# Optimization experiments

Hardware: AMD Instinct MI355X
Metric: run time of the kernel (lower is better)

## Reference

```python
import jax, jax.numpy as jnp
import numpy as np

B, S, D = 4, 2048, 512
H, DK = 16, 32  # n_heads, d_k == d_v == args.mid_dim


def setup_inputs() -> dict:
    key = jax.random.key(0)
    ks = jax.random.split(key, 9)
    s = 0.02
    return {
        "x": jax.random.normal(ks[0], (B, S, D), dtype=jnp.float32),
        "Wq": jax.random.normal(ks[1], (D, H * DK), dtype=jnp.float32) * s,
        "bq": jnp.zeros((H * DK,), dtype=jnp.float32),
        "Wk": jax.random.normal(ks[2], (D, H * DK), dtype=jnp.float32) * s,
        "bk": jnp.zeros((H * DK,), dtype=jnp.float32),
        "Wv": jax.random.normal(ks[3], (D, H * DK), dtype=jnp.float32) * s,
        "bv": jnp.zeros((H * DK,), dtype=jnp.float32),
        "Wo": jax.random.normal(ks[4], (H * DK, D), dtype=jnp.float32) * s,
        "bo": jnp.zeros((D,), dtype=jnp.float32),
        "mask_border": 64,
    }


def reference(x, Wq, bq, Wk, bk, Wv, bv, Wo, bo, mask_border):
    b, s, d = x.shape
    # band mask: tril(ones, border) * triu(ones, -border) == 1 where |i-j| <= border
    i = jnp.arange(s)
    band = (jnp.abs(i[:, None] - i[None, :]) <= mask_border).astype(x.dtype)  # [S,S]

    q = (x @ Wq + bq).reshape(b, s, H, DK)
    k = (x @ Wk + bk).reshape(b, s, H, DK)
    v = (x @ Wv + bv).reshape(b, s, H, DK)

    scale = 1.0 / jnp.sqrt(jnp.asarray(DK, x.dtype))
    # float attn_mask is ADDED to scores (PatchTST-style _ScaledDotProductAttention)
    scores = jnp.einsum("bihd,bjhd->bhij", q, k) * scale + band[None, None]
    attn = jax.nn.softmax(scores, axis=-1)
    o = jnp.einsum("bhij,bjhd->bihd", attn, v).reshape(b, s, H * DK)
    out_1 = o @ Wo + bo  # [B,S,D]

    # reconstruction score + quantiles (side stats; do not feed returned tensor)
    rec_score = jnp.mean((out_1 - x) ** 2, axis=2)  # [B,S]
    q1, q2, q3 = jnp.quantile(rec_score, jnp.array([0.25, 0.5, 0.75], rec_score.dtype), axis=-1)
    del q1, q2, q3

    # tmp = out_1 - x; out_1 = x + tmp  (identity); module returns out_1
    return out_1
```

## Files before the change

### kernel.cpp

```cpp
#include <hip/hip_runtime.h>
#include <hip/hip_bf16.h>

#define B_ 4
#define S_ 2048
#define D_ 512
#define H_ 16
#define DK_ 32
#define MS_ 8192

typedef unsigned short u16;
typedef __attribute__((ext_vector_type(4))) unsigned short u16x4;
typedef __attribute__((ext_vector_type(8))) short bf16x8;
typedef __attribute__((ext_vector_type(4))) float f32x4;

__device__ __forceinline__ u16 f2b(float f) {
    union { float f; unsigned u; } uf; uf.f = f;
    unsigned u = uf.u;
    unsigned r = u + 0x7fffu + ((u >> 16) & 1u);
    return (u16)(r >> 16);
}

__device__ __forceinline__ unsigned cvt_pk_bf16(float lo, float hi) {
    unsigned r;
    asm("v_cvt_pk_bf16_f32 %0, %1, %2" : "=v"(r) : "v"(lo), "v"(hi));
    return r;
}

__device__ __forceinline__ void gload16(const u16* src, u16* dst) {
    __builtin_amdgcn_global_load_lds(
        (const __attribute__((address_space(1))) unsigned int*)src,
        (__attribute__((address_space(3))) unsigned int*)dst, 16, 0, 0);
}

__global__ void cast_f32_to_bf16(const float* __restrict__ in, u16* __restrict__ out, int n4) {
    int i = blockIdx.x * blockDim.x + threadIdx.x;
    if (i >= n4) return;
    f32x4 v = *(const f32x4*)(in + (size_t)i * 4);
    u16x4 o;
    o[0] = f2b(v[0]); o[1] = f2b(v[1]); o[2] = f2b(v[2]); o[3] = f2b(v[3]);
    *(u16x4*)(out + (size_t)i * 4) = o;
}

__global__ void transpose_cast(const float* __restrict__ Wq, const float* __restrict__ Wk,
                               const float* __restrict__ Wv, const float* __restrict__ Wo,
                               u16* __restrict__ out) {
    const int z = blockIdx.z;
    const float* W = (z == 0) ? Wq : (z == 1) ? Wk : (z == 2) ? Wv : Wo;
    u16* O = out + (size_t)z * D_ * D_;
    __shared__ float T[32][33];
    const int n0 = blockIdx.x * 32, k0 = blockIdx.y * 32;
    const int tx = threadIdx.x & 31, ty = threadIdx.x >> 5;
#pragma unroll
    for (int i = 0; i < 4; i++) {
        int row = ty + 8 * i;
        T[tx][row] = W[(size_t)(k0 + row) * D_ + n0 + tx];
    }
    __syncthreads();
#pragma unroll
    for (int i = 0; i < 4; i++) {
        int row = ty + 8 * i;
        O[(size_t)(n0 + row) * D_ + k0 + tx] = f2b(T[row][tx]);
    }
}

__launch_bounds__(256)
__global__ void gemm_qkv(const u16* __restrict__ Xb, const u16* __restrict__ WT,
                         const float* __restrict__ bq, const float* __restrict__ bk, const float* __restrict__ bv,
                         u16* __restrict__ Qw, u16* __restrict__ Kw, u16* __restrict__ Vw) {
    const int which = blockIdx.z;
    const u16* Wt = WT + (size_t)which * D_ * D_;
    const float* bias = (which == 0) ? bq : (which == 1) ? bk : bv;
    u16* Out = (which == 0) ? Qw : (which == 1) ? Kw : Vw;

    __shared__ __attribute__((aligned(16))) u16 As[128][64];
    __shared__ __attribute__((aligned(16))) u16 Bs[128][64];

    const int tid = threadIdx.x;
    const int lane = tid & 63, w = tid >> 6;
    const int wr = w >> 1, wc = w & 1;
    const int g = lane >> 4, c = lane & 15;
    const int bm0 = blockIdx.y * 128, bn0 = blockIdx.x * 128;

    const int trow = tid >> 3;
    const int tcg = (tid & 7) ^ (trow & 7);
    const u16* gA = Xb + (size_t)(bm0 + trow) * D_ + 8 * tcg;
    const u16* gB = Wt + (size_t)(bn0 + trow) * D_ + 8 * tcg;

    f32x4 acc[4][4];
#pragma unroll
    for (int i = 0; i < 4; i++)
#pragma unroll
        for (int j = 0; j < 4; j++) acc[i][j] = (f32x4)0.0f;

    for (int k0 = 0; k0 < D_; k0 += 64) {
#pragma unroll
        for (int i = 0; i < 4; i++) {
            gload16(gA + (size_t)(32 * i) * D_ + k0, &As[0][0] + 512 * w + 2048 * i);
            gload16(gB + (size_t)(32 * i) * D_ + k0, &Bs[0][0] + 512 * w + 2048 * i);
        }
        __syncthreads();
#pragma unroll
        for (int kk = 0; kk < 2; kk++) {
            bf16x8 a[4], b[4];
#pragma unroll
            for (int mi = 0; mi < 4; mi++)
                a[mi] = *(const bf16x8*)&As[wr * 64 + 16 * mi + c][8 * ((4 * kk + g) ^ (c & 7))];
#pragma unroll
            for (int ni = 0; ni < 4; ni++)
                b[ni] = *(const bf16x8*)&Bs[wc * 64 + 16 * ni + c][8 * ((4 * kk + g) ^ (c & 7))];
#pragma unroll
            for (int mi = 0; mi < 4; mi++)
#pragma unroll
                for (int ni = 0; ni < 4; ni++)
                    acc[mi][ni] = __builtin_amdgcn_mfma_f32_16x16x32_bf16(a[mi], b[ni], acc[mi][ni], 0, 0, 0);
        }
        __syncthreads();
    }
#pragma unroll
    for (int mi = 0; mi < 4; mi++)
#pragma unroll
        for (int ni = 0; ni < 4; ni++)
#pragma unroll
            for (int r = 0; r < 4; r++) {
                int m = bm0 + wr * 64 + 16 * mi + 4 * g + r;
                int n = bn0 + wc * 64 + 16 * ni + c;
                float v = acc[mi][ni][r] + bias[n];
                int b = m >> 11, s = m & 2047;
                int h = n >> 5, dk = n & 31;
                Out[(((size_t)(b * H_ + h) * S_) + s) * DK_ + dk] = f2b(v);
            }
}

__launch_bounds__(512)
__global__ void attn_kernel(const u16* __restrict__ Q, const u16* __restrict__ K,
                            const u16* __restrict__ V, u16* __restrict__ O,
                            const int* __restrict__ mbp) {
    const int border = *mbp;
    const unsigned b2u = (unsigned)(2 * border);
    const int bh = blockIdx.x;
    const int q0 = blockIdx.y * 128;
    const int tid = threadIdx.x;
    const int lane = tid & 63;
    const int w = __builtin_amdgcn_readfirstlane(tid >> 6);
    const int g = lane >> 4, c = lane & 15;

    __shared__ __attribute__((aligned(16))) u16 Ks[128][32];
    __shared__ __attribute__((aligned(16))) u16 Vt0[32][68];
    __shared__ __attribute__((aligned(16))) u16 Vt1[32][68];

    const u16* Qbh = Q + (size_t)bh * S_ * DK_;
    const u16* Kbh = K + (size_t)bh * S_ * DK_;
    const u16* Vbh = V + (size_t)bh * S_ * DK_;

    const int qw0 = q0 + w * 16;
    const int qi = qw0 + c;
    const bf16x8 qf = *(const bf16x8*)&Qbh[(size_t)qi * DK_ + 8 * g];

    f32x4 accO[2];
    accO[0] = (f32x4)0.0f; accO[1] = (f32x4)0.0f;
    float lr0 = 0.f, lr1 = 0.f, lr2 = 0.f, lr3 = 0.f;

    const float C1 = (float)(1.4426950408889634 / 5.656854249492381);
    const float C2 = 1.4426950408889634f;

    const int skk = tid >> 3;
    const int sc4 = (tid & 7) << 2;
    const int srow = 32 * ((skk >> 2) & 1) + 16 * ((skk >> 5) & 1) + (((skk >> 3) & 3) << 2) + (skk & 3);

    for (int kv0 = 0; kv0 < S_; kv0 += 128) {
        *(u16x4*)&Ks[srow][sc4]      = *(const u16x4*)&Kbh[(size_t)(kv0 + skk) * DK_ + sc4];
        *(u16x4*)&Ks[64 + srow][sc4] = *(const u16x4*)&Kbh[(size_t)(kv0 + 64 + skk) * DK_ + sc4];
        u16x4 va = *(const u16x4*)&Vbh[(size_t)(kv0 + skk) * DK_ + sc4];
        u16x4 vb = *(const u16x4*)&Vbh[(size_t)(kv0 + 64 + skk) * DK_ + sc4];
#pragma unroll
        for (int j = 0; j < 4; j++) {
            Vt0[sc4 + j][skk] = va[j];
            Vt1[sc4 + j][skk] = vb[j];
        }
        __syncthreads();

        union { unsigned u[4]; bf16x8 v; } pb[4];

        {
            f32x4 sf[4];
#pragma unroll
            for (int ct = 0; ct < 4; ct++) {
                const bf16x8 kf = *(const bf16x8*)&Ks[16 * ct + c][8 * g];
                sf[ct] = __builtin_amdgcn_mfma_f32_16x16x32_bf16(kf, qf, (f32x4)0.0f, 0, 0, 0);
            }
            const int kvs = kv0;
            float e[4][4];
            const bool aOut = (qw0 > kvs + 63 + border) || (qw0 + 15 + border < kvs);
            const bool aIn  = (qw0 + 15 <= kvs + border) && (kvs + 63 <= qw0 + border);
            if (aOut) {
#pragma unroll
                for (int ct = 0; ct < 4; ct++)
#pragma unroll
                    for (int r = 0; r < 4; r++)
                        e[ct][r] = __builtin_amdgcn_exp2f(sf[ct][r] * C1);
            } else if (aIn) {
#pragma unroll
                for (int ct = 0; ct < 4; ct++)
#pragma unroll
                    for (int r = 0; r < 4; r++)
                        e[ct][r] = __builtin_amdgcn_exp2f(__builtin_fmaf(sf[ct][r], C1, C2));
            } else {
                const int qb = qi + border - kvs;
#pragma unroll
                for (int ct = 0; ct < 4; ct++) {
                    const int k0l = 32 * (ct & 1) + 8 * g + 4 * (ct >> 1);
#pragma unroll
                    for (int r = 0; r < 4; r++) {
                        float a = ((unsigned)(qb - (k0l + r)) <= b2u) ? C2 : 0.0f;
                        e[ct][r] = __builtin_amdgcn_exp2f(__builtin_fmaf(sf[ct][r], C1, a));
                    }
                }
            }
#pragma unroll
            for (int ct = 0; ct < 4; ct++) {
                lr0 += e[ct][0]; lr1 += e[ct][1]; lr2 += e[ct][2]; lr3 += e[ct][3];
            }
            pb[0].u[0] = cvt_pk_bf16(e[0][0], e[0][1]);
            pb[0].u[1] = cvt_pk_bf16(e[0][2], e[0][3]);
            pb[0].u[2] = cvt_pk_bf16(e[2][0], e[2][1]);
            pb[0].u[3] = cvt_pk_bf16(e[2][2], e[2][3]);
            pb[1].u[0] = cvt_pk_bf16(e[1][0], e[1][1]);
            pb[1].u[1] = cvt_pk_bf16(e[1][2], e[1][3]);
            pb[1].u[2] = cvt_pk_bf16(e[3][0], e[3][1]);
            pb[1].u[3] = cvt_pk_bf16(e[3][2], e[3][3]);
        }

        {
            f32x4 sf[4];
#pragma unroll
            for (int ct = 0; ct < 4; ct++) {
                const bf16x8 kf = *(const bf16x8*)&Ks[64 + 16 * ct + c][8 * g];
                sf[ct] = __builtin_amdgcn_mfma_f32_16x16x32_bf16(kf, qf, (f32x4)0.0f, 0, 0, 0);
            }
            const int kvs = kv0 + 64;
            float e[4][4];
            const bool aOut = (qw0 > kvs + 63 + border) || (qw0 + 15 + border < kvs);
            const bool aIn  = (qw0 + 15 <= kvs + border) && (kvs + 63 <= qw0 + border);
            if (aOut) {
#pragma unroll
                for (int ct = 0; ct < 4; ct++)
#pragma unroll
                    for (int r = 0; r < 4; r++)
                        e[ct][r] = __builtin_amdgcn_exp2f(sf[ct][r] * C1);
            } else if (aIn) {
#pragma unroll
                for (int ct = 0; ct < 4; ct++)
#pragma unroll
                    for (int r = 0; r < 4; r++)
                        e[ct][r] = __builtin_amdgcn_exp2f(__builtin_fmaf(sf[ct][r], C1, C2));
            } else {
                const int qb = qi + border - kvs;
#pragma unroll
                for (int ct = 0; ct < 4; ct++) {
                    const int k0l = 32 * (ct & 1) + 8 * g + 4 * (ct >> 1);
#pragma unroll
                    for (int r = 0; r < 4; r++) {
                        float a = ((unsigned)(qb - (k0l + r)) <= b2u) ? C2 : 0.0f;
                        e[ct][r] = __builtin_amdgcn_exp2f(__builtin_fmaf(sf[ct][r], C1, a));
                    }
                }
            }
#pragma unroll
            for (int ct = 0; ct < 4; ct++) {
                lr0 += e[ct][0]; lr1 += e[ct][1]; lr2 += e[ct][2]; lr3 += e[ct][3];
            }
            pb[2].u[0] = cvt_pk_bf16(e[0][0], e[0][1]);
            pb[2].u[1] = cvt_pk_bf16(e[0][2], e[0][3]);
            pb[2].u[2] = cvt_pk_bf16(e[2][0], e[2][1]);
            pb[2].u[3] = cvt_pk_bf16(e[2][2], e[2][3]);
            pb[3].u[0] = cvt_pk_bf16(e[1][0], e[1][1]);
            pb[3].u[1] = cvt_pk_bf16(e[1][2], e[1][3]);
            pb[3].u[2] = cvt_pk_bf16(e[3][0], e[3][1]);
            pb[3].u[3] = cvt_pk_bf16(e[3][2], e[3][3]);
        }

#pragma unroll
        for (int t = 0; t < 2; t++) {
            union { u16x4 h[2]; bf16x8 v; } vf;
            vf.h[0] = *(const u16x4*)&Vt0[16 * t + c][8 * g];
            vf.h[1] = *(const u16x4*)&Vt0[16 * t + c][8 * g + 4];
            accO[t] = __builtin_amdgcn_mfma_f32_16x16x32_bf16(vf.v, pb[0].v, accO[t], 0, 0, 0);
            vf.h[0] = *(const u16x4*)&Vt0[16 * t + c][32 + 8 * g];
            vf.h[1] = *(const u16x4*)&Vt0[16 * t + c][32 + 8 * g + 4];
            accO[t] = __builtin_amdgcn_mfma_f32_16x16x32_bf16(vf.v, pb[1].v, accO[t], 0, 0, 0);
            vf.h[0] = *(const u16x4*)&Vt1[16 * t + c][8 * g];
            vf.h[1] = *(const u16x4*)&Vt1[16 * t + c][8 * g + 4];
            accO[t] = __builtin_amdgcn_mfma_f32_16x16x32_bf16(vf.v, pb[2].v, accO[t], 0, 0, 0);
            vf.h[0] = *(const u16x4*)&Vt1[16 * t + c][32 + 8 * g];
            vf.h[1] = *(const u16x4*)&Vt1[16 * t + c][32 + 8 * g + 4];
            accO[t] = __builtin_amdgcn_mfma_f32_16x16x32_bf16(vf.v, pb[3].v, accO[t], 0, 0, 0);
        }
        __syncthreads();
    }

    float l = ((lr0 + lr1) + (lr2 + lr3));
    l += __shfl_xor(l, 16);
    l += __shfl_xor(l, 32);
    const float linv = 1.0f / l;

    const int b = bh >> 4, h = bh & 15;
#pragma unroll
    for (int t = 0; t < 2; t++) {
        u16x4 o4;
#pragma unroll
        for (int r = 0; r < 4; r++) o4[r] = f2b(accO[t][r] * linv);
        *(u16x4*)&O[((size_t)(b * S_ + qi) * H_ + h) * DK_ + 16 * t + 4 * g] = o4;
    }
}

__launch_bounds__(256)
__global__ void gemm_out(const u16* __restrict__ Ob, const u16* __restrict__ WoT,
                         const float* __restrict__ bo, float* __restrict__ out) {
    __shared__ __attribute__((aligned(16))) u16 As[128][64];
    __shared__ __attribute__((aligned(16))) u16 Bs[128][64];

    const int tid = threadIdx.x;
    const int lane = tid & 63, w = tid >> 6;
    const int wr = w >> 1, wc = w & 1;
    const int g = lane >> 4, c = lane & 15;
    const int bm0 = blockIdx.y * 128, bn0 = blockIdx.x * 128;

    const int trow = tid >> 3;
    const int tcg = (tid & 7) ^ (trow & 7);
    const u16* gA = Ob + (size_t)(bm0 + trow) * D_ + 8 * tcg;
    const u16* gB = WoT + (size_t)(bn0 + trow) * D_ + 8 * tcg;

    f32x4 acc[4][4];
#pragma unroll
    for (int i = 0; i < 4; i++)
#pragma unroll
        for (int j = 0; j < 4; j++) acc[i][j] = (f32x4)0.0f;

    for (int k0 = 0; k0 < D_; k0 += 64) {
#pragma unroll
        for (int i = 0; i < 4; i++) {
            gload16(gA + (size_t)(32 * i) * D_ + k0, &As[0][0] + 512 * w + 2048 * i);
            gload16(gB + (size_t)(32 * i) * D_ + k0, &Bs[0][0] + 512 * w + 2048 * i);
        }
        __syncthreads();
#pragma unroll
        for (int kk = 0; kk < 2; kk++) {
            bf16x8 a[4], b[4];
#pragma unroll
            for (int mi = 0; mi < 4; mi++)
                a[mi] = *(const bf16x8*)&As[wr * 64 + 16 * mi + c][8 * ((4 * kk + g) ^ (c & 7))];
#pragma unroll
            for (int ni = 0; ni < 4; ni++)
                b[ni] = *(const bf16x8*)&Bs[wc * 64 + 16 * ni + c][8 * ((4 * kk + g) ^ (c & 7))];
#pragma unroll
            for (int mi = 0; mi < 4; mi++)
#pragma unroll
                for (int ni = 0; ni < 4; ni++)
                    acc[mi][ni] = __builtin_amdgcn_mfma_f32_16x16x32_bf16(a[mi], b[ni], acc[mi][ni], 0, 0, 0);
        }
        __syncthreads();
    }
#pragma unroll
    for (int mi = 0; mi < 4; mi++)
#pragma unroll
        for (int ni = 0; ni < 4; ni++)
#pragma unroll
            for (int r = 0; r < 4; r++) {
                int m = bm0 + wr * 64 + 16 * mi + 4 * g + r;
                int n = bn0 + wc * 64 + 16 * ni + c;
                out[(size_t)m * D_ + n] = acc[mi][ni][r] + bo[n];
            }
}

extern "C" void kernel_launch(void* const* d_in, const int* in_sizes, int n_in,
                              void* d_out, int out_size, void* d_ws, size_t ws_size,
                              hipStream_t stream) {
    const float* x  = (const float*)d_in[0];
    const float* Wq = (const float*)d_in[1];
    const float* bq = (const float*)d_in[2];
    const float* Wk = (const float*)d_in[3];
    const float* bk = (const float*)d_in[4];
    const float* Wv = (const float*)d_in[5];
    const float* bv = (const float*)d_in[6];
    const float* Wo = (const float*)d_in[7];
    const float* bo = (const float*)d_in[8];
    const int* mb   = (const int*)d_in[9];
    float* out = (float*)d_out;

    char* p = (char*)d_ws;
    u16* xb = (u16*)p; p += (size_t)MS_ * D_ * 2;
    u16* wt = (u16*)p; p += (size_t)4 * D_ * D_ * 2;
    u16* qw = (u16*)p; p += (size_t)MS_ * D_ * 2;
    u16* kw = (u16*)p; p += (size_t)MS_ * D_ * 2;
    u16* vw = (u16*)p; p += (size_t)MS_ * D_ * 2;
    u16* ow = (u16*)p; p += (size_t)MS_ * D_ * 2;

    cast_f32_to_bf16<<<4096, 256, 0, stream>>>(x, xb, MS_ * D_ / 4);
    transpose_cast<<<dim3(16, 16, 4), 256, 0, stream>>>(Wq, Wk, Wv, Wo, wt);

    gemm_qkv<<<dim3(4, 64, 3), 256, 0, stream>>>(xb, wt, bq, bk, bv, qw, kw, vw);
    attn_kernel<<<dim3(64, 16), 512, 0, stream>>>(qw, kw, vw, ow, mb);
    gemm_out<<<dim3(4, 64), 256, 0, stream>>>(ow, wt + (size_t)3 * D_ * D_, bo, out);
}
```

Baseline: 116.5 us.

## Process two query tiles per wave, fold softmax scale into Q, sum rows via MFMA

Each attention wave now handles 32 queries instead of 16, so every K/V tile loaded into LDS is reused across twice as many queries, and the grid is halved. The softmax scale times log2(e) is folded into the Q projection epilogue, which removes a multiply per score. Row sums are computed with an MFMA against a ones vector instead of scalar adds and cross-lane shuffles. In exchange, register pressure per wave goes up, there are half as many blocks (512) to fill the GPU, and the row sum is now taken over bf16-rounded probabilities.

```diff
diff --git a/kernel.cpp b/kernel.cpp
--- a/kernel.cpp
+++ b/kernel.cpp
@@ -12,6 +12,8 @@
 typedef __attribute__((ext_vector_type(4))) unsigned short u16x4;
 typedef __attribute__((ext_vector_type(8))) short bf16x8;
 typedef __attribute__((ext_vector_type(4))) float f32x4;
+
+union pbu { unsigned u[4]; bf16x8 v; };
 
 __device__ __forceinline__ u16 f2b(float f) {
     union { float f; unsigned u; } uf; uf.f = f;
@@ -71,6 +73,7 @@
     const u16* Wt = WT + (size_t)which * D_ * D_;
     const float* bias = (which == 0) ? bq : (which == 1) ? bk : bv;
     u16* Out = (which == 0) ? Qw : (which == 1) ? Kw : Vw;
+    const float oscale = (which == 0) ? (float)(1.4426950408889634 / 5.656854249492381) : 1.0f;
 
     __shared__ __attribute__((aligned(16))) u16 As[128][64];
     __shared__ __attribute__((aligned(16))) u16 Bs[128][64];
@@ -124,7 +127,7 @@
             for (int r = 0; r < 4; r++) {
                 int m = bm0 + wr * 64 + 16 * mi + 4 * g + r;
                 int n = bn0 + wc * 64 + 16 * ni + c;
-                float v = acc[mi][ni][r] + bias[n];
+                float v = (acc[mi][ni][r] + bias[n]) * oscale;
                 int b = m >> 11, s = m & 2047;
                 int h = n >> 5, dk = n & 31;
                 Out[(((size_t)(b * H_ + h) * S_) + s) * DK_ + dk] = f2b(v);
@@ -138,34 +141,106 @@
     const int border = *mbp;
     const unsigned b2u = (unsigned)(2 * border);
     const int bh = blockIdx.x;
-    const int q0 = blockIdx.y * 128;
+    const int q0 = blockIdx.y * 256;
     const int tid = threadIdx.x;
     const int lane = tid & 63;
     const int w = __builtin_amdgcn_readfirstlane(tid >> 6);
     const int g = lane >> 4, c = lane & 15;
 
     __shared__ __attribute__((aligned(16))) u16 Ks[128][32];
-    __shared__ __attribute__((aligned(16))) u16 Vt0[32][68];
-    __shared__ __attribute__((aligned(16))) u16 Vt1[32][68];
+    __shared__ __attribute__((aligned(16))) u16 Vt[2][32][68];
 
     const u16* Qbh = Q + (size_t)bh * S_ * DK_;
     const u16* Kbh = K + (size_t)bh * S_ * DK_;
     const u16* Vbh = V + (size_t)bh * S_ * DK_;
 
-    const int qw0 = q0 + w * 16;
-    const int qi = qw0 + c;
-    const bf16x8 qf = *(const bf16x8*)&Qbh[(size_t)qi * DK_ + 8 * g];
-
-    f32x4 accO[2];
-    accO[0] = (f32x4)0.0f; accO[1] = (f32x4)0.0f;
-    float lr0 = 0.f, lr1 = 0.f, lr2 = 0.f, lr3 = 0.f;
-
-    const float C1 = (float)(1.4426950408889634 / 5.656854249492381);
+    const int qw0 = q0 + w * 32;
+    const int qiA = qw0 + c;
+    const int qiB = qw0 + 16 + c;
+    const bf16x8 qfA = *(const bf16x8*)&Qbh[(size_t)qiA * DK_ + 8 * g];
+    const bf16x8 qfB = *(const bf16x8*)&Qbh[(size_t)qiB * DK_ + 8 * g];
+
+    f32x4 accO[2][2];
+    f32x4 accL[2];
+#pragma unroll
+    for (int i = 0; i < 2; i++) { accO[i][0] = (f32x4)0.0f; accO[i][1] = (f32x4)0.0f; accL[i] = (f32x4)0.0f; }
+
     const float C2 = 1.4426950408889634f;
+
+    union { u16x4 h[2]; bf16x8 v; } ones;
+#pragma unroll
+    for (int j = 0; j < 4; j++) { ones.h[0][j] = 0x3F80; ones.h[1][j] = 0x3F80; }
 
     const int skk = tid >> 3;
     const int sc4 = (tid & 7) << 2;
     const int srow = 32 * ((skk >> 2) & 1) + 16 * ((skk >> 5) & 1) + (((skk >> 3) & 3) << 2) + (skk & 3);
+
+    auto sm_pack = [&](const f32x4* sf, int qs0, int qiv, int kvs, pbu* pb) {
+        float e[4][4];
+        const bool aOut = (qs0 > kvs + 63 + border) || (qs0 + 15 + border < kvs);
+        const bool aIn  = (qs0 + 15 <= kvs + border) && (kvs + 63 <= qs0 + border);
+        if (aOut) {
+#pragma unroll
+            for (int ct = 0; ct < 4; ct++)
+#pragma unroll
+                for (int r = 0; r < 4; r++)
+                    e[ct][r] = __builtin_amdgcn_exp2f(sf[ct][r]);
+        } else if (aIn) {
+#pragma unroll
+            for (int ct = 0; ct < 4; ct++)
+#pragma unroll
+                for (int r = 0; r < 4; r++)
+                    e[ct][r] = __builtin_amdgcn_exp2f(sf[ct][r] + C2);
+        } else {
+            const int qb = qiv + border - kvs;
+#pragma unroll
+            for (int ct = 0; ct < 4; ct++) {
+                const int k0l = 32 * (ct & 1) + 8 * g + 4 * (ct >> 1);
+#pragma unroll
+                for (int r = 0; r < 4; r++) {
+                    float a = ((unsigned)(qb - (k0l + r)) <= b2u) ? C2 : 0.0f;
+                    e[ct][r] = __builtin_amdgcn_exp2f(sf[ct][r] + a);
+                }
+            }
+        }
+        pb[0].u[0] = cvt_pk_bf16(e[0][0], e[0][1]);
+        pb[0].u[1] = cvt_pk_bf16(e[0][2], e[0][3]);
+        pb[0].u[2] = cvt_pk_bf16(e[2][0], e[2][1]);
+        pb[0].u[3] = cvt_pk_bf16(e[2][2], e[2][3]);
+        pb[1].u[0] = cvt_pk_bf16(e[1][0], e[1][1]);
+        pb[1].u[1] = cvt_pk_bf16(e[1][2], e[1][3]);
+        pb[1].u[2] = cvt_pk_bf16(e[3][0], e[3][1]);
+        pb[1].u[3] = cvt_pk_bf16(e[3][2], e[3][3]);
+    };
+
+    auto do_sub = [&](int sub, int kvs) {
+        f32x4 sA[4], sB[4];
+#pragma unroll
+        for (int ct = 0; ct < 4; ct++) {
+            const bf16x8 kf = *(const bf16x8*)&Ks[sub * 64 + 16 * ct + c][8 * g];
+            sA[ct] = __builtin_amdgcn_mfma_f32_16x16x32_bf16(kf, qfA, (f32x4)0.0f, 0, 0, 0);
+            sB[ct] = __builtin_amdgcn_mfma_f32_16x16x32_bf16(kf, qfB, (f32x4)0.0f, 0, 0, 0);
+        }
+        pbu pA[2], pB[2];
+        sm_pack(sA, qw0, qiA, kvs, pA);
+        sm_pack(sB, qw0 + 16, qiB, kvs, pB);
+#pragma unroll
+        for (int t2 = 0; t2 < 2; t2++) {
+#pragma unroll
+            for (int ksl = 0; ksl < 2; ksl++) {
+                union { u16x4 h[2]; bf16x8 v; } vf;
+                vf.h[0] = *(const u16x4*)&Vt[sub][16 * t2 + c][32 * ksl + 8 * g];
+                vf.h[1] = *(const u16x4*)&Vt[sub][16 * t2 + c][32 * ksl + 8 * g + 4];
+                accO[0][t2] = __builtin_amdgcn_mfma_f32_16x16x32_bf16(vf.v, pA[ksl].v, accO[0][t2], 0, 0, 0);
+                accO[1][t2] = __builtin_amdgcn_mfma_f32_16x16x32_bf16(vf.v, pB[ksl].v, accO[1][t2], 0, 0, 0);
+            }
+        }
+#pragma unroll
+        for (int ksl = 0; ksl < 2; ksl++) {
+            accL[0] = __builtin_amdgcn_mfma_f32_16x16x32_bf16(ones.v, pA[ksl].v, accL[0], 0, 0, 0);
+            accL[1] = __builtin_amdgcn_mfma_f32_16x16x32_bf16(ones.v, pB[ksl].v, accL[1], 0, 0, 0);
+        }
+    };
 
     for (int kv0 = 0; kv0 < S_; kv0 += 128) {
         *(u16x4*)&Ks[srow][sc4]      = *(const u16x4*)&Kbh[(size_t)(kv0 + skk) * DK_ + sc4];
@@ -174,142 +249,30 @@
         u16x4 vb = *(const u16x4*)&Vbh[(size_t)(kv0 + 64 + skk) * DK_ + sc4];
 #pragma unroll
         for (int j = 0; j < 4; j++) {
-            Vt0[sc4 + j][skk] = va[j];
-            Vt1[sc4 + j][skk] = vb[j];
-        }
-        __syncthreads();
-
-        union { unsigned u[4]; bf16x8 v; } pb[4];
-
-        {
-            f32x4 sf[4];
-#pragma unroll
-            for (int ct = 0; ct < 4; ct++) {
-                const bf16x8 kf = *(const bf16x8*)&Ks[16 * ct + c][8 * g];
-                sf[ct] = __builtin_amdgcn_mfma_f32_16x16x32_bf16(kf, qf, (f32x4)0.0f, 0, 0, 0);
-            }
-            const int kvs = kv0;
-            float e[4][4];
-            const bool aOut = (qw0 > kvs + 63 + border) || (qw0 + 15 + border < kvs);
-            const bool aIn  = (qw0 + 15 <= kvs + border) && (kvs + 63 <= qw0 + border);
-            if (aOut) {
-#pragma unroll
-                for (int ct = 0; ct < 4; ct++)
-#pragma unroll
-                    for (int r = 0; r < 4; r++)
-                        e[ct][r] = __builtin_amdgcn_exp2f(sf[ct][r] * C1);
-            } else if (aIn) {
-#pragma unroll
-                for (int ct = 0; ct < 4; ct++)
-#pragma unroll
-                    for (int r = 0; r < 4; r++)
-                        e[ct][r] = __builtin_amdgcn_exp2f(__builtin_fmaf(sf[ct][r], C1, C2));
-            } else {
-                const int qb = qi + border - kvs;
-#pragma unroll
-                for (int ct = 0; ct < 4; ct++) {
-                    const int k0l = 32 * (ct & 1) + 8 * g + 4 * (ct >> 1);
-#pragma unroll
-                    for (int r = 0; r < 4; r++) {
-                        float a = ((unsigned)(qb - (k0l + r)) <= b2u) ? C2 : 0.0f;
-                        e[ct][r] = __builtin_amdgcn_exp2f(__builtin_fmaf(sf[ct][r], C1, a));
-                    }
-                }
-            }
-#pragma unroll
-            for (int ct = 0; ct < 4; ct++) {
-                lr0 += e[ct][0]; lr1 += e[ct][1]; lr2 += e[ct][2]; lr3 += e[ct][3];
-            }
-            pb[0].u[0] = cvt_pk_bf16(e[0][0], e[0][1]);
-            pb[0].u[1] = cvt_pk_bf16(e[0][2], e[0][3]);
-            pb[0].u[2] = cvt_pk_bf16(e[2][0], e[2][1]);
-            pb[0].u[3] = cvt_pk_bf16(e[2][2], e[2][3]);
-            pb[1].u[0] = cvt_pk_bf16(e[1][0], e[1][1]);
-            pb[1].u[1] = cvt_pk_bf16(e[1][2], e[1][3]);
-            pb[1].u[2] = cvt_pk_bf16(e[3][0], e[3][1]);
-            pb[1].u[3] = cvt_pk_bf16(e[3][2], e[3][3]);
-        }
-
-        {
-            f32x4 sf[4];
-#pragma unroll
-            for (int ct = 0; ct < 4; ct++) {
-                const bf16x8 kf = *(const bf16x8*)&Ks[64 + 16 * ct + c][8 * g];
-                sf[ct] = __builtin_amdgcn_mfma_f32_16x16x32_bf16(kf, qf, (f32x4)0.0f, 0, 0, 0);
-            }
-            const int kvs = kv0 + 64;
-            float e[4][4];
-            const bool aOut = (qw0 > kvs + 63 + border) || (qw0 + 15 + border < kvs);
-            const bool aIn  = (qw0 + 15 <= kvs + border) && (kvs + 63 <= qw0 + border);
-            if (aOut) {
-#pragma unroll
-                for (int ct = 0; ct < 4; ct++)
-#pragma unroll
-                    for (int r = 0; r < 4; r++)
-                        e[ct][r] = __builtin_amdgcn_exp2f(sf[ct][r] * C1);
-            } else if (aIn) {
-#pragma unroll
-                for (int ct = 0; ct < 4; ct++)
-#pragma unroll
-                    for (int r = 0; r < 4; r++)
-                        e[ct][r] = __builtin_amdgcn_exp2f(__builtin_fmaf(sf[ct][r], C1, C2));
-            } else {
-                const int qb = qi + border - kvs;
-#pragma unroll
-                for (int ct = 0; ct < 4; ct++) {
-                    const int k0l = 32 * (ct & 1) + 8 * g + 4 * (ct >> 1);
-#pragma unroll
-                    for (int r = 0; r < 4; r++) {
-                        float a = ((unsigned)(qb - (k0l + r)) <= b2u) ? C2 : 0.0f;
-                        e[ct][r] = __builtin_amdgcn_exp2f(__builtin_fmaf(sf[ct][r], C1, a));
-                    }
-                }
-            }
-#pragma unroll
-            for (int ct = 0; ct < 4; ct++) {
-                lr0 += e[ct][0]; lr1 += e[ct][1]; lr2 += e[ct][2]; lr3 += e[ct][3];
-            }
-            pb[2].u[0] = cvt_pk_bf16(e[0][0], e[0][1]);
-            pb[2].u[1] = cvt_pk_bf16(e[0][2], e[0][3]);
-            pb[2].u[2] = cvt_pk_bf16(e[2][0], e[2][1]);
-            pb[2].u[3] = cvt_pk_bf16(e[2][2], e[2][3]);
-            pb[3].u[0] = cvt_pk_bf16(e[1][0], e[1][1]);
-            pb[3].u[1] = cvt_pk_bf16(e[1][2], e[1][3]);
-            pb[3].u[2] = cvt_pk_bf16(e[3][0], e[3][1]);
-            pb[3].u[3] = cvt_pk_bf16(e[3][2], e[3][3]);
-        }
-
-#pragma unroll
-        for (int t = 0; t < 2; t++) {
-            union { u16x4 h[2]; bf16x8 v; } vf;
-            vf.h[0] = *(const u16x4*)&Vt0[16 * t + c][8 * g];
-            vf.h[1] = *(const u16x4*)&Vt0[16 * t + c][8 * g + 4];
-            accO[t] = __builtin_amdgcn_mfma_f32_16x16x32_bf16(vf.v, pb[0].v, accO[t], 0, 0, 0);
-            vf.h[0] = *(const u16x4*)&Vt0[16 * t + c][32 + 8 * g];
-            vf.h[1] = *(const u16x4*)&Vt0[16 * t + c][32 + 8 * g + 4];
-            accO[t] = __builtin_amdgcn_mfma_f32_16x16x32_bf16(vf.v, pb[1].v, accO[t], 0, 0, 0);
-            vf.h[0] = *(const u16x4*)&Vt1[16 * t + c][8 * g];
-            vf.h[1] = *(const u16x4*)&Vt1[16 * t + c][8 * g + 4];
-            accO[t] = __builtin_amdgcn_mfma_f32_16x16x32_bf16(vf.v, pb[2].v, accO[t], 0, 0, 0);
-            vf.h[0] = *(const u16x4*)&Vt1[16 * t + c][32 + 8 * g];
-            vf.h[1] = *(const u16x4*)&Vt1[16 * t + c][32 + 8 * g + 4];
-            accO[t] = __builtin_amdgcn_mfma_f32_16x16x32_bf16(vf.v, pb[3].v, accO[t], 0, 0, 0);
-        }
-        __syncthreads();
-    }
-
-    float l = ((lr0 + lr1) + (lr2 + lr3));
-    l += __shfl_xor(l, 16);
-    l += __shfl_xor(l, 32);
-    const float linv = 1.0f / l;
+            Vt[0][sc4 + j][skk] = va[j];
+            Vt[1][sc4 + j][skk] = vb[j];
+        }
+        __syncthreads();
+
+        do_sub(0, kv0);
+        do_sub(1, kv0 + 64);
+
+        __syncthreads();
+    }
 
     const int b = bh >> 4, h = bh & 15;
-#pragma unroll
-    for (int t = 0; t < 2; t++) {
-        u16x4 o4;
-#pragma unroll
-        for (int r = 0; r < 4; r++) o4[r] = f2b(accO[t][r] * linv);
-        *(u16x4*)&O[((size_t)(b * S_ + qi) * H_ + h) * DK_ + 16 * t + 4 * g] = o4;
+    const float linvA = 1.0f / accL[0][0];
+    const float linvB = 1.0f / accL[1][0];
+#pragma unroll
+    for (int t2 = 0; t2 < 2; t2++) {
+        u16x4 oA, oB;
+#pragma unroll
+        for (int r = 0; r < 4; r++) {
+            oA[r] = f2b(accO[0][t2][r] * linvA);
+            oB[r] = f2b(accO[1][t2][r] * linvB);
+        }
+        *(u16x4*)&O[((size_t)(b * S_ + qiA) * H_ + h) * DK_ + 16 * t2 + 4 * g] = oA;
+        *(u16x4*)&O[((size_t)(b * S_ + qiB) * H_ + h) * DK_ + 16 * t2 + 4 * g] = oB;
     }
 }
 
@@ -399,6 +362,6 @@
     transpose_cast<<<dim3(16, 16, 4), 256, 0, stream>>>(Wq, Wk, Wv, Wo, wt);
 
     gemm_qkv<<<dim3(4, 64, 3), 256, 0, stream>>>(xb, wt, bq, bk, bv, qw, kw, vw);
-    attn_kernel<<<dim3(64, 16), 512, 0, stream>>>(qw, kw, vw, ow, mb);
+    attn_kernel<<<dim3(64, 8), 512, 0, stream>>>(qw, kw, vw, ow, mb);
     gemm_out<<<dim3(4, 64), 256, 0, stream>>>(ow, wt + (size_t)3 * D_ * D_, bo, out);
 }
```

Measured after the change: 101.4 us. 12.9% less time.
